# Optimization experiments

Measured on AMD Instinct MI355X. Metric: run time of the kernel, lower is better.

The kernel has to match this reference:

```python
import jax, jax.numpy as jnp
import numpy as np
import math

N_HEAD = 16

def _rope(x):
    # x: [B, H, T, D], D even; interleaved-pair rotation as in the torch code
    B, H, T, D = x.shape
    theta = 10000.0 ** (-2.0 * jnp.arange(D // 2, dtype=x.dtype) / D)  # [D/2]
    pos = jnp.arange(T, dtype=x.dtype)[:, None]                        # [T,1]
    ang = pos * theta[None, :]                                          # [T, D/2]
    sin, cos = jnp.sin(ang), jnp.cos(ang)
    x1, x2 = x[..., ::2], x[..., 1::2]
    x1r = x1 * cos - x2 * sin
    x2r = x1 * sin + x2 * cos
    # re-interleave
    out = jnp.stack([x1r, x2r], axis=-1).reshape(B, H, T, D)
    return out

def setup_inputs() -> dict:
    key = jax.random.key(0)
    ks = jax.random.split(key, 3)
    B, T, C = 4, 2048, 1024
    x = jax.random.normal(ks[0], (B, T, C), dtype=jnp.float32)
    W_qkv = jax.random.normal(ks[1], (C, 3 * C), dtype=jnp.float32) * (1.0 / math.sqrt(C))
    b_qkv = jnp.zeros((3 * C,), dtype=jnp.float32)
    W_proj = jax.random.normal(ks[2], (C, C), dtype=jnp.float32) * (1.0 / math.sqrt(C))
    b_proj = jnp.zeros((C,), dtype=jnp.float32)
    return {"x": x, "W_qkv": W_qkv, "b_qkv": b_qkv, "W_proj": W_proj, "b_proj": b_proj}

def reference(x, W_qkv, b_qkv, W_proj, b_proj):
    B, T, C = x.shape
    H = N_HEAD
    D = C // H
    qkv = x @ W_qkv + b_qkv                      # [B,T,3C]
    q, k, v = jnp.split(qkv, 3, axis=-1)
    def to_heads(t):
        return t.reshape(B, T, H, D).transpose(0, 2, 1, 3)  # [B,H,T,D]
    q, k, v = to_heads(q), to_heads(k), to_heads(v)
    q = _rope(q)
    k = _rope(k)
    att = jnp.einsum('bhqd,bhkd->bhqk', q, k) * (1.0 / math.sqrt(D))
    mask = jnp.tril(jnp.ones((T, T), dtype=bool))
    att = jnp.where(mask[None, None, :, :], att, -jnp.inf)
    att = jax.nn.softmax(att, axis=-1)
    y = jnp.einsum('bhqk,bhkd->bhqd', att, v)    # [B,H,T,D]
    y = y.transpose(0, 2, 1, 3).reshape(B, T, C)
    return y @ W_proj + b_proj
```

## Files before the change

### kernel.cpp

```cpp
#include <hip/hip_runtime.h>
#include <cstddef>

#define B_DIM 4
#define T_DIM 2048
#define C_DIM 1024
#define H_DIM 16
#define D_DIM 64
#define C3_DIM 3072

typedef __attribute__((ext_vector_type(8))) _Float16 f16x8;
typedef __attribute__((ext_vector_type(4))) _Float16 f16x4;
typedef __attribute__((ext_vector_type(4))) float f32x4;

typedef const __attribute__((address_space(1))) unsigned int* gptr_t;
typedef __attribute__((address_space(3))) unsigned int* lptr_t;

#define QSCALE 0.180336850073f
#define NTHETA 0.41524101186f

__global__ __launch_bounds__(256) void prep(
    const float* __restrict__ x, _Float16* __restrict__ xh,
    const float* __restrict__ Wq, _Float16* __restrict__ Wqt,
    const float* __restrict__ Wp, _Float16* __restrict__ Wpt)
{
    __shared__ float tile[64][65];
    const int z = blockIdx.x, tid = threadIdx.x;

    if (z < 8192) {
        size_t i = (size_t)z * 1024 + tid * 4;
        float4 v = *(const float4*)&x[i];
        f16x4 o = { (_Float16)v.x, (_Float16)v.y, (_Float16)v.z, (_Float16)v.w };
        *(f16x4*)&xh[i] = o;
        return;
    }

    const float* W;
    _Float16* Wt;
    int N, idx;
    if (z < 8960) { W = Wq; Wt = Wqt; N = C3_DIM; idx = z - 8192; }
    else          { W = Wp; Wt = Wpt; N = C_DIM;  idx = z - 8960; }
    const int K = C_DIM;
    const int nblk = N / 64;
    const int n0 = (idx % nblk) * 64, k0 = (idx / nblk) * 64;

    const int tx = tid & 15, ty = tid >> 4;
#pragma unroll
    for (int it = 0; it < 4; ++it) {
        int r = it * 16 + ty;
        *(float4*)&tile[r][tx * 4] =
            *(const float4*)&W[(size_t)(k0 + r) * N + n0 + tx * 4];
    }
    __syncthreads();
    int c = tid >> 2, t0 = (tid & 3) * 16;
    __align__(16) _Float16 tmp[16];
#pragma unroll
    for (int j = 0; j < 16; ++j) tmp[j] = (_Float16)tile[t0 + j][c];
    _Float16* o = Wt + (size_t)(n0 + c) * K + k0 + t0;
    *(f16x8*)o = *(f16x8*)&tmp[0];
    *(f16x8*)(o + 8) = *(f16x8*)&tmp[8];
}

__global__ __launch_bounds__(256) void gemm_qkv(
    const _Float16* __restrict__ A, const _Float16* __restrict__ Bt,
    const float* __restrict__ bias,
    _Float16* __restrict__ Qb, _Float16* __restrict__ Kb, _Float16* __restrict__ Vt)
{
    __shared__ __align__(16) _Float16 Af[8][64][8];
    __shared__ __align__(16) _Float16 Bf[8][64][8];
    const int tid = threadIdx.x;
    const int lane = tid & 63, w = tid >> 6;
    const int lm = lane & 15, lq = lane >> 4;
    const int wm = w >> 1, wn = w & 1;
    const int m0 = blockIdx.y * 128, n0 = blockIdx.x * 128;
    const int K = C_DIM;

    const _Float16* a0 = A + (size_t)(m0 + w * 32 + lm) * K + lq * 8;
    const _Float16* a1 = a0 + (size_t)16 * K;
    const _Float16* b0 = Bt + (size_t)(n0 + w * 32 + lm) * K + lq * 8;
    const _Float16* b1 = b0 + (size_t)16 * K;

    f32x4 acc[4][4];
#pragma unroll
    for (int i = 0; i < 4; ++i)
#pragma unroll
        for (int j = 0; j < 4; ++j) acc[i][j] = (f32x4){0.f, 0.f, 0.f, 0.f};

    const bool is_v = (n0 >= 2 * C_DIM);

    if (!is_v) {
        for (int k0 = 0; k0 < K; k0 += 32) {
            __syncthreads();
            __builtin_amdgcn_global_load_lds((gptr_t)(const void*)(a0 + k0),
                (lptr_t)(void*)&Af[w * 2 + 0][0][0], 16, 0, 0);
            __builtin_amdgcn_global_load_lds((gptr_t)(const void*)(a1 + k0),
                (lptr_t)(void*)&Af[w * 2 + 1][0][0], 16, 0, 0);
            __builtin_amdgcn_global_load_lds((gptr_t)(const void*)(b0 + k0),
                (lptr_t)(void*)&Bf[w * 2 + 0][0][0], 16, 0, 0);
            __builtin_amdgcn_global_load_lds((gptr_t)(const void*)(b1 + k0),
                (lptr_t)(void*)&Bf[w * 2 + 1][0][0], 16, 0, 0);
            __syncthreads();
            f16x8 av[4], bv[4];
#pragma unroll
            for (int i = 0; i < 4; ++i) {
                av[i] = *(const f16x8*)&Af[wm * 4 + i][lane][0];
                bv[i] = *(const f16x8*)&Bf[wn * 4 + i][lane][0];
            }
#pragma unroll
            for (int i = 0; i < 4; ++i)
#pragma unroll
                for (int j = 0; j < 4; ++j)
                    acc[i][j] = __builtin_amdgcn_mfma_f32_16x16x32_f16(
                        bv[j], av[i], acc[i][j], 0, 0, 0);
        }

        const bool is_q = (n0 < C_DIM);
        const float scale = is_q ? QSCALE : 1.0f;
        _Float16* dstbase = is_q ? Qb : Kb;
#pragma unroll
        for (int j = 0; j < 4; ++j) {
            int col = n0 + wn * 64 + j * 16 + lq * 4;
            int d0 = col & 63;
            int h = (col & (C_DIM - 1)) >> 6;
            float4 b4 = *(const float4*)&bias[col];
            float th0 = exp2f(-NTHETA * (float)(d0 >> 1));
            float th1 = exp2f(-NTHETA * (float)((d0 >> 1) + 1));
#pragma unroll
            for (int i = 0; i < 4; ++i) {
                int tg = m0 + wm * 64 + i * 16 + lm;
                int bb = tg >> 11, tl = tg & (T_DIM - 1);
                float v0 = acc[i][j][0] + b4.x;
                float v1 = acc[i][j][1] + b4.y;
                float v2 = acc[i][j][2] + b4.z;
                float v3 = acc[i][j][3] + b4.w;
                float s0, c0, s1, c1;
                __sincosf((float)tl * th0, &s0, &c0);
                __sincosf((float)tl * th1, &s1, &c1);
                f16x4 o = { (_Float16)((v0 * c0 - v1 * s0) * scale),
                            (_Float16)((v0 * s0 + v1 * c0) * scale),
                            (_Float16)((v2 * c1 - v3 * s1) * scale),
                            (_Float16)((v2 * s1 + v3 * c1) * scale) };
                *(f16x4*)&dstbase[((size_t)(bb * 16 + h) * T_DIM + tl) * 64 + d0] = o;
            }
        }
    } else {
        for (int k0 = 0; k0 < K; k0 += 32) {
            __syncthreads();
            __builtin_amdgcn_global_load_lds((gptr_t)(const void*)(a0 + k0),
                (lptr_t)(void*)&Af[w * 2 + 0][0][0], 16, 0, 0);
            __builtin_amdgcn_global_load_lds((gptr_t)(const void*)(a1 + k0),
                (lptr_t)(void*)&Af[w * 2 + 1][0][0], 16, 0, 0);
            __builtin_amdgcn_global_load_lds((gptr_t)(const void*)(b0 + k0),
                (lptr_t)(void*)&Bf[w * 2 + 0][0][0], 16, 0, 0);
            __builtin_amdgcn_global_load_lds((gptr_t)(const void*)(b1 + k0),
                (lptr_t)(void*)&Bf[w * 2 + 1][0][0], 16, 0, 0);
            __syncthreads();
            f16x8 av[4], bv[4];
#pragma unroll
            for (int i = 0; i < 4; ++i) {
                av[i] = *(const f16x8*)&Af[wm * 4 + i][lane][0];
                bv[i] = *(const f16x8*)&Bf[wn * 4 + i][lane][0];
            }
#pragma unroll
            for (int i = 0; i < 4; ++i)
#pragma unroll
                for (int j = 0; j < 4; ++j)
                    acc[i][j] = __builtin_amdgcn_mfma_f32_16x16x32_f16(
                        av[i], bv[j], acc[i][j], 0, 0, 0);
        }

#pragma unroll
        for (int i = 0; i < 4; ++i) {
            int t4 = m0 + wm * 64 + i * 16 + lq * 4;
            int bb = t4 >> 11, tl = t4 & (T_DIM - 1);
#pragma unroll
            for (int j = 0; j < 4; ++j) {
                int col = n0 + wn * 64 + j * 16 + lm;
                int dfull = col - 2 * C_DIM;
                int h = dfull >> 6, d = dfull & 63;
                float bc = bias[col];
                f16x4 o = { (_Float16)(acc[i][j][0] + bc),
                            (_Float16)(acc[i][j][1] + bc),
                            (_Float16)(acc[i][j][2] + bc),
                            (_Float16)(acc[i][j][3] + bc) };
                *(f16x4*)&Vt[((size_t)(bb * 16 + h) * 64 + d) * T_DIM + tl] = o;
            }
        }
    }
}

template <bool OUT_HALF>
__global__ __launch_bounds__(256) void gemm_bt(
    const _Float16* __restrict__ A, const _Float16* __restrict__ Bt,
    const float* __restrict__ bias, void* __restrict__ Cout,
    int M, int N, int K)
{
    __shared__ __align__(16) _Float16 Af[8][64][8];
    __shared__ __align__(16) _Float16 Bf[8][64][8];
    const int tid = threadIdx.x;
    const int lane = tid & 63, w = tid >> 6;
    const int lm = lane & 15, lq = lane >> 4;
    const int wm = w >> 1, wn = w & 1;
    const int m0 = blockIdx.y * 128, n0 = blockIdx.x * 128;

    const _Float16* a0 = A + (size_t)(m0 + w * 32 + lm) * K + lq * 8;
    const _Float16* a1 = a0 + (size_t)16 * K;
    const _Float16* b0 = Bt + (size_t)(n0 + w * 32 + lm) * K + lq * 8;
    const _Float16* b1 = b0 + (size_t)16 * K;

    f32x4 acc[4][4];
#pragma unroll
    for (int i = 0; i < 4; ++i)
#pragma unroll
        for (int j = 0; j < 4; ++j) acc[i][j] = (f32x4){0.f, 0.f, 0.f, 0.f};

    for (int k0 = 0; k0 < K; k0 += 32) {
        __syncthreads();
        __builtin_amdgcn_global_load_lds((gptr_t)(const void*)(a0 + k0),
            (lptr_t)(void*)&Af[w * 2 + 0][0][0], 16, 0, 0);
        __builtin_amdgcn_global_load_lds((gptr_t)(const void*)(a1 + k0),
            (lptr_t)(void*)&Af[w * 2 + 1][0][0], 16, 0, 0);
        __builtin_amdgcn_global_load_lds((gptr_t)(const void*)(b0 + k0),
            (lptr_t)(void*)&Bf[w * 2 + 0][0][0], 16, 0, 0);
        __builtin_amdgcn_global_load_lds((gptr_t)(const void*)(b1 + k0),
            (lptr_t)(void*)&Bf[w * 2 + 1][0][0], 16, 0, 0);
        __syncthreads();

        f16x8 av[4], bv[4];
#pragma unroll
        for (int i = 0; i < 4; ++i) {
            av[i] = *(const f16x8*)&Af[wm * 4 + i][lane][0];
            bv[i] = *(const f16x8*)&Bf[wn * 4 + i][lane][0];
        }
#pragma unroll
        for (int i = 0; i < 4; ++i)
#pragma unroll
            for (int j = 0; j < 4; ++j)
                acc[i][j] = __builtin_amdgcn_mfma_f32_16x16x32_f16(
                    bv[j], av[i], acc[i][j], 0, 0, 0);
    }

#pragma unroll
    for (int i = 0; i < 4; ++i) {
        size_t row = (size_t)(m0 + wm * 64 + i * 16 + lm);
#pragma unroll
        for (int j = 0; j < 4; ++j) {
            int col = n0 + wn * 64 + j * 16 + lq * 4;
            float4 b4 = *(const float4*)&bias[col];
            float v0 = acc[i][j][0] + b4.x;
            float v1 = acc[i][j][1] + b4.y;
            float v2 = acc[i][j][2] + b4.z;
            float v3 = acc[i][j][3] + b4.w;
            if (OUT_HALF) {
                f16x4 o = { (_Float16)v0, (_Float16)v1, (_Float16)v2, (_Float16)v3 };
                *(f16x4*)&((_Float16*)Cout)[row * N + col] = o;
            } else {
                float4 o = make_float4(v0, v1, v2, v3);
                *(float4*)&((float*)Cout)[row * N + col] = o;
            }
        }
    }
}

__global__ __launch_bounds__(256) void attn_mfma(
    const _Float16* __restrict__ Qb, const _Float16* __restrict__ Kb,
    const _Float16* __restrict__ Vt, _Float16* __restrict__ yb)
{
    __shared__ __align__(16) _Float16 Kf[8][64][8];
    __shared__ __align__(16) _Float16 Vf[8][64][8];
    __shared__ __align__(16) _Float16 Pb[4][16][72];

    const int tid = threadIdx.x;
    const int bh = blockIdx.x;
    const int qt = 31 - blockIdx.y;
    const int b = bh >> 4, h = bh & 15;
    const int lane = tid & 63, w = tid >> 6;
    const int m = lane & 15, qq = lane >> 4;

    const _Float16* qrow = Qb +
        ((size_t)bh * T_DIM + qt * 64 + w * 16 + m) * D_DIM + qq * 8;
    f16x8 qreg[2];
    qreg[0] = *(const f16x8*)qrow;
    qreg[1] = *(const f16x8*)(qrow + 32);

    float m_i = -1e30f, l_i = 0.f;
    f32x4 acc[4];
#pragma unroll
    for (int db = 0; db < 4; ++db) acc[db] = (f32x4){0.f, 0.f, 0.f, 0.f};

    const _Float16* kg0 = Kb + (size_t)bh * T_DIM * D_DIM +
                          (size_t)(w * 16 + m) * D_DIM + qq * 8;
    const _Float16* vg0 = Vt + (size_t)bh * D_DIM * T_DIM +
                          (size_t)(w * 16 + m) * T_DIM + qq * 8;

    f16x8 kr0 = *(const f16x8*)(kg0);
    f16x8 kr1 = *(const f16x8*)(kg0 + 32);
    f16x8 vr0 = *(const f16x8*)(vg0);
    f16x8 vr1 = *(const f16x8*)(vg0 + 32);

    for (int kt = 0; kt <= qt; ++kt) {
        __syncthreads();
        *(f16x8*)&Kf[w * 2 + 0][lane][0] = kr0;
        *(f16x8*)&Kf[w * 2 + 1][lane][0] = kr1;
        *(f16x8*)&Vf[w * 2 + 0][lane][0] = vr0;
        *(f16x8*)&Vf[w * 2 + 1][lane][0] = vr1;
        __syncthreads();

        int ktn = (kt < qt) ? kt + 1 : kt;
        kr0 = *(const f16x8*)(kg0 + (size_t)ktn * 64 * D_DIM);
        kr1 = *(const f16x8*)(kg0 + (size_t)ktn * 64 * D_DIM + 32);
        vr0 = *(const f16x8*)(vg0 + ktn * 64);
        vr1 = *(const f16x8*)(vg0 + ktn * 64 + 32);

        f32x4 sv[4];
#pragma unroll
        for (int nb = 0; nb < 4; ++nb) {
            f32x4 s = (f32x4){0.f, 0.f, 0.f, 0.f};
            s = __builtin_amdgcn_mfma_f32_16x16x32_f16(
                *(const f16x8*)&Kf[nb * 2 + 0][lane][0], qreg[0], s, 0, 0, 0);
            s = __builtin_amdgcn_mfma_f32_16x16x32_f16(
                *(const f16x8*)&Kf[nb * 2 + 1][lane][0], qreg[1], s, 0, 0, 0);
            sv[nb] = s;
        }

        if (kt == qt) {
            int qlocal = w * 16 + m;
#pragma unroll
            for (int nb = 0; nb < 4; ++nb) {
                int tb = nb * 16 + qq * 4;
#pragma unroll
                for (int r = 0; r < 4; ++r)
                    if (tb + r > qlocal) sv[nb][r] = -1e30f;
            }
        }

        float mt0 = fmaxf(fmaxf(sv[0][0], sv[0][1]), fmaxf(sv[0][2], sv[0][3]));
        float mt1 = fmaxf(fmaxf(sv[1][0], sv[1][1]), fmaxf(sv[1][2], sv[1][3]));
        float mt2 = fmaxf(fmaxf(sv[2][0], sv[2][1]), fmaxf(sv[2][2], sv[2][3]));
        float mt3 = fmaxf(fmaxf(sv[3][0], sv[3][1]), fmaxf(sv[3][2], sv[3][3]));
        float mt = fmaxf(fmaxf(mt0, mt1), fmaxf(mt2, mt3));
        mt = fmaxf(mt, __shfl_xor(mt, 16));
        mt = fmaxf(mt, __shfl_xor(mt, 32));
        float mnew = fmaxf(m_i, mt);
        float alpha = exp2f(m_i - mnew);
        float ll = 0.f;
#pragma unroll
        for (int nb = 0; nb < 4; ++nb) {
            float p0 = exp2f(sv[nb][0] - mnew);
            float p1 = exp2f(sv[nb][1] - mnew);
            float p2 = exp2f(sv[nb][2] - mnew);
            float p3 = exp2f(sv[nb][3] - mnew);
            sv[nb][0] = p0; sv[nb][1] = p1; sv[nb][2] = p2; sv[nb][3] = p3;
            ll += (p0 + p1) + (p2 + p3);
        }
        ll += __shfl_xor(ll, 16);
        ll += __shfl_xor(ll, 32);
        l_i = l_i * alpha + ll;
        m_i = mnew;
#pragma unroll
        for (int db = 0; db < 4; ++db) {
            acc[db][0] *= alpha; acc[db][1] *= alpha;
            acc[db][2] *= alpha; acc[db][3] *= alpha;
        }

#pragma unroll
        for (int nb = 0; nb < 4; ++nb) {
            f16x4 pv = { (_Float16)sv[nb][0], (_Float16)sv[nb][1],
                         (_Float16)sv[nb][2], (_Float16)sv[nb][3] };
            *(f16x4*)&Pb[w][m][nb * 16 + qq * 4] = pv;
        }

        f16x8 pf0 = *(const f16x8*)&Pb[w][m][0 * 32 + qq * 8];
        f16x8 pf1 = *(const f16x8*)&Pb[w][m][1 * 32 + qq * 8];

#pragma unroll
        for (int db = 0; db < 4; ++db) {
            acc[db] = __builtin_amdgcn_mfma_f32_16x16x32_f16(
                *(const f16x8*)&Vf[db * 2 + 0][lane][0], pf0, acc[db], 0, 0, 0);
            acc[db] = __builtin_amdgcn_mfma_f32_16x16x32_f16(
                *(const f16x8*)&Vf[db * 2 + 1][lane][0], pf1, acc[db], 0, 0, 0);
        }
    }

    float inv = 1.0f / l_i;
    _Float16* yrow = yb + (size_t)(b * T_DIM + qt * 64 + w * 16 + m) * C_DIM +
                     h * D_DIM + qq * 4;
#pragma unroll
    for (int db = 0; db < 4; ++db) {
        f16x4 o = { (_Float16)(acc[db][0] * inv), (_Float16)(acc[db][1] * inv),
                    (_Float16)(acc[db][2] * inv), (_Float16)(acc[db][3] * inv) };
        *(f16x4*)(yrow + db * 16) = o;
    }
}

extern "C" void kernel_launch(void* const* d_in, const int* in_sizes, int n_in,
                              void* d_out, int out_size, void* d_ws, size_t ws_size,
                              hipStream_t stream)
{
    const float* x     = (const float*)d_in[0];
    const float* Wqkv  = (const float*)d_in[1];
    const float* bqkv  = (const float*)d_in[2];
    const float* Wproj = (const float*)d_in[3];
    const float* bproj = (const float*)d_in[4];
    float* out = (float*)d_out;

    char* ws = (char*)d_ws;
    _Float16* xh  = (_Float16*)(ws);
    _Float16* yh  = (_Float16*)(ws + 16777216ull);
    _Float16* Qb  = (_Float16*)(ws + 33554432ull);
    _Float16* Kb  = (_Float16*)(ws + 50331648ull);
    _Float16* Vt  = (_Float16*)(ws + 67108864ull);
    _Float16* Wqt = (_Float16*)(ws + 83886080ull);
    _Float16* Wpt = (_Float16*)(ws + 90177536ull);

    dim3 blk(256);

    prep<<<dim3(9216), blk, 0, stream>>>(x, xh, Wqkv, Wqt, Wproj, Wpt);

    gemm_qkv<<<dim3(C3_DIM / 128, (B_DIM * T_DIM) / 128), blk, 0, stream>>>(
        xh, Wqt, bqkv, Qb, Kb, Vt);

    attn_mfma<<<dim3(B_DIM * H_DIM, T_DIM / 64), blk, 0, stream>>>(
        Qb, Kb, Vt, yh);

    gemm_bt<false><<<dim3(C_DIM / 128, (B_DIM * T_DIM) / 128), blk, 0, stream>>>(
        yh, Wpt, bproj, out, B_DIM * T_DIM, C_DIM, C_DIM);
}
```

Baseline: 319.1 us.

## Double-buffer LDS tiles and widen K-step to 64 in QKV and projection GEMMs

Both GEMM kernels now stage two K-slices of 32 (64 total) per iteration into a double-buffered LDS array. The next tile's global-to-LDS loads are issued before computing on the current buffer, and there is one barrier per 64-wide step instead of two per 32-wide step. The goal is to hide global load latency behind MFMA work and cut synchronisation overhead. LDS use per block grows fourfold (to 64 KB total), which may lower occupancy.

```diff
diff --git a/kernel.cpp b/kernel.cpp
--- a/kernel.cpp
+++ b/kernel.cpp
@@ -60,13 +60,55 @@
     *(f16x8*)(o + 8) = *(f16x8*)&tmp[8];
 }
 
+#define STAGE8(BUF, KK)                                                       \
+    do {                                                                      \
+        __builtin_amdgcn_global_load_lds((gptr_t)(const void*)(ag + (KK)),    \
+            (lptr_t)(void*)&Af[BUF][0][w * 2 + 0][0][0], 16, 0, 0);           \
+        __builtin_amdgcn_global_load_lds((gptr_t)(const void*)(ag + (KK) + 16 * K), \
+            (lptr_t)(void*)&Af[BUF][0][w * 2 + 1][0][0], 16, 0, 0);           \
+        __builtin_amdgcn_global_load_lds((gptr_t)(const void*)(ag + (KK) + 32), \
+            (lptr_t)(void*)&Af[BUF][1][w * 2 + 0][0][0], 16, 0, 0);           \
+        __builtin_amdgcn_global_load_lds((gptr_t)(const void*)(ag + (KK) + 32 + 16 * K), \
+            (lptr_t)(void*)&Af[BUF][1][w * 2 + 1][0][0], 16, 0, 0);           \
+        __builtin_amdgcn_global_load_lds((gptr_t)(const void*)(bg + (KK)),    \
+            (lptr_t)(void*)&Bf[BUF][0][w * 2 + 0][0][0], 16, 0, 0);           \
+        __builtin_amdgcn_global_load_lds((gptr_t)(const void*)(bg + (KK) + 16 * K), \
+            (lptr_t)(void*)&Bf[BUF][0][w * 2 + 1][0][0], 16, 0, 0);           \
+        __builtin_amdgcn_global_load_lds((gptr_t)(const void*)(bg + (KK) + 32), \
+            (lptr_t)(void*)&Bf[BUF][1][w * 2 + 0][0][0], 16, 0, 0);           \
+        __builtin_amdgcn_global_load_lds((gptr_t)(const void*)(bg + (KK) + 32 + 16 * K), \
+            (lptr_t)(void*)&Bf[BUF][1][w * 2 + 1][0][0], 16, 0, 0);           \
+    } while (0)
+
+#define COMPUTE64(CUR, SWAPPED)                                               \
+    do {                                                                      \
+        _Pragma("unroll")                                                     \
+        for (int s = 0; s < 2; ++s) {                                         \
+            f16x8 av[4], bv[4];                                               \
+            _Pragma("unroll")                                                 \
+            for (int i = 0; i < 4; ++i) {                                     \
+                av[i] = *(const f16x8*)&Af[CUR][s][wm * 4 + i][lane][0];      \
+                bv[i] = *(const f16x8*)&Bf[CUR][s][wn * 4 + i][lane][0];      \
+            }                                                                 \
+            _Pragma("unroll")                                                 \
+            for (int i = 0; i < 4; ++i)                                       \
+                _Pragma("unroll")                                             \
+                for (int j = 0; j < 4; ++j)                                   \
+                    acc[i][j] = (SWAPPED)                                     \
+                        ? __builtin_amdgcn_mfma_f32_16x16x32_f16(             \
+                              bv[j], av[i], acc[i][j], 0, 0, 0)               \
+                        : __builtin_amdgcn_mfma_f32_16x16x32_f16(             \
+                              av[i], bv[j], acc[i][j], 0, 0, 0);              \
+        }                                                                     \
+    } while (0)
+
 __global__ __launch_bounds__(256) void gemm_qkv(
     const _Float16* __restrict__ A, const _Float16* __restrict__ Bt,
     const float* __restrict__ bias,
     _Float16* __restrict__ Qb, _Float16* __restrict__ Kb, _Float16* __restrict__ Vt)
 {
-    __shared__ __align__(16) _Float16 Af[8][64][8];
-    __shared__ __align__(16) _Float16 Bf[8][64][8];
+    __shared__ __align__(16) _Float16 Af[2][2][8][64][8];
+    __shared__ __align__(16) _Float16 Bf[2][2][8][64][8];
     const int tid = threadIdx.x;
     const int lane = tid & 63, w = tid >> 6;
     const int lm = lane & 15, lq = lane >> 4;
@@ -74,10 +116,8 @@
     const int m0 = blockIdx.y * 128, n0 = blockIdx.x * 128;
     const int K = C_DIM;
 
-    const _Float16* a0 = A + (size_t)(m0 + w * 32 + lm) * K + lq * 8;
-    const _Float16* a1 = a0 + (size_t)16 * K;
-    const _Float16* b0 = Bt + (size_t)(n0 + w * 32 + lm) * K + lq * 8;
-    const _Float16* b1 = b0 + (size_t)16 * K;
+    const _Float16* ag = A + (size_t)(m0 + w * 32 + lm) * K + lq * 8;
+    const _Float16* bg = Bt + (size_t)(n0 + w * 32 + lm) * K + lq * 8;
 
     f32x4 acc[4][4];
 #pragma unroll
@@ -88,30 +128,16 @@
     const bool is_v = (n0 >= 2 * C_DIM);
 
     if (!is_v) {
-        for (int k0 = 0; k0 < K; k0 += 32) {
+        STAGE8(0, 0);
+        __syncthreads();
+        int cur = 0;
+        for (int kt = 0; kt < K / 64 - 1; ++kt) {
+            STAGE8(cur ^ 1, (kt + 1) * 64);
+            COMPUTE64(cur, true);
             __syncthreads();
-            __builtin_amdgcn_global_load_lds((gptr_t)(const void*)(a0 + k0),
-                (lptr_t)(void*)&Af[w * 2 + 0][0][0], 16, 0, 0);
-            __builtin_amdgcn_global_load_lds((gptr_t)(const void*)(a1 + k0),
-                (lptr_t)(void*)&Af[w * 2 + 1][0][0], 16, 0, 0);
-            __builtin_amdgcn_global_load_lds((gptr_t)(const void*)(b0 + k0),
-                (lptr_t)(void*)&Bf[w * 2 + 0][0][0], 16, 0, 0);
-            __builtin_amdgcn_global_load_lds((gptr_t)(const void*)(b1 + k0),
-                (lptr_t)(void*)&Bf[w * 2 + 1][0][0], 16, 0, 0);
-            __syncthreads();
-            f16x8 av[4], bv[4];
-#pragma unroll
-            for (int i = 0; i < 4; ++i) {
-                av[i] = *(const f16x8*)&Af[wm * 4 + i][lane][0];
-                bv[i] = *(const f16x8*)&Bf[wn * 4 + i][lane][0];
-            }
-#pragma unroll
-            for (int i = 0; i < 4; ++i)
-#pragma unroll
-                for (int j = 0; j < 4; ++j)
-                    acc[i][j] = __builtin_amdgcn_mfma_f32_16x16x32_f16(
-                        bv[j], av[i], acc[i][j], 0, 0, 0);
-        }
+            cur ^= 1;
+        }
+        COMPUTE64(cur, true);
 
         const bool is_q = (n0 < C_DIM);
         const float scale = is_q ? QSCALE : 1.0f;
@@ -143,30 +169,16 @@
             }
         }
     } else {
-        for (int k0 = 0; k0 < K; k0 += 32) {
+        STAGE8(0, 0);
+        __syncthreads();
+        int cur = 0;
+        for (int kt = 0; kt < K / 64 - 1; ++kt) {
+            STAGE8(cur ^ 1, (kt + 1) * 64);
+            COMPUTE64(cur, false);
             __syncthreads();
-            __builtin_amdgcn_global_load_lds((gptr_t)(const void*)(a0 + k0),
-                (lptr_t)(void*)&Af[w * 2 + 0][0][0], 16, 0, 0);
-            __builtin_amdgcn_global_load_lds((gptr_t)(const void*)(a1 + k0),
-                (lptr_t)(void*)&Af[w * 2 + 1][0][0], 16, 0, 0);
-            __builtin_amdgcn_global_load_lds((gptr_t)(const void*)(b0 + k0),
-                (lptr_t)(void*)&Bf[w * 2 + 0][0][0], 16, 0, 0);
-            __builtin_amdgcn_global_load_lds((gptr_t)(const void*)(b1 + k0),
-                (lptr_t)(void*)&Bf[w * 2 + 1][0][0], 16, 0, 0);
-            __syncthreads();
-            f16x8 av[4], bv[4];
-#pragma unroll
-            for (int i = 0; i < 4; ++i) {
-                av[i] = *(const f16x8*)&Af[wm * 4 + i][lane][0];
-                bv[i] = *(const f16x8*)&Bf[wn * 4 + i][lane][0];
-            }
-#pragma unroll
-            for (int i = 0; i < 4; ++i)
-#pragma unroll
-                for (int j = 0; j < 4; ++j)
-                    acc[i][j] = __builtin_amdgcn_mfma_f32_16x16x32_f16(
-                        av[i], bv[j], acc[i][j], 0, 0, 0);
-        }
+            cur ^= 1;
+        }
+        COMPUTE64(cur, false);
 
 #pragma unroll
         for (int i = 0; i < 4; ++i) {
@@ -194,18 +206,16 @@
     const float* __restrict__ bias, void* __restrict__ Cout,
     int M, int N, int K)
 {
-    __shared__ __align__(16) _Float16 Af[8][64][8];
-    __shared__ __align__(16) _Float16 Bf[8][64][8];
+    __shared__ __align__(16) _Float16 Af[2][2][8][64][8];
+    __shared__ __align__(16) _Float16 Bf[2][2][8][64][8];
     const int tid = threadIdx.x;
     const int lane = tid & 63, w = tid >> 6;
     const int lm = lane & 15, lq = lane >> 4;
     const int wm = w >> 1, wn = w & 1;
     const int m0 = blockIdx.y * 128, n0 = blockIdx.x * 128;
 
-    const _Float16* a0 = A + (size_t)(m0 + w * 32 + lm) * K + lq * 8;
-    const _Float16* a1 = a0 + (size_t)16 * K;
-    const _Float16* b0 = Bt + (size_t)(n0 + w * 32 + lm) * K + lq * 8;
-    const _Float16* b1 = b0 + (size_t)16 * K;
+    const _Float16* ag = A + (size_t)(m0 + w * 32 + lm) * K + lq * 8;
+    const _Float16* bg = Bt + (size_t)(n0 + w * 32 + lm) * K + lq * 8;
 
     f32x4 acc[4][4];
 #pragma unroll
@@ -213,31 +223,16 @@
 #pragma unroll
         for (int j = 0; j < 4; ++j) acc[i][j] = (f32x4){0.f, 0.f, 0.f, 0.f};
 
-    for (int k0 = 0; k0 < K; k0 += 32) {
+    STAGE8(0, 0);
+    __syncthreads();
+    int cur = 0;
+    for (int kt = 0; kt < K / 64 - 1; ++kt) {
+        STAGE8(cur ^ 1, (kt + 1) * 64);
+        COMPUTE64(cur, true);
         __syncthreads();
-        __builtin_amdgcn_global_load_lds((gptr_t)(const void*)(a0 + k0),
-            (lptr_t)(void*)&Af[w * 2 + 0][0][0], 16, 0, 0);
-        __builtin_amdgcn_global_load_lds((gptr_t)(const void*)(a1 + k0),
-            (lptr_t)(void*)&Af[w * 2 + 1][0][0], 16, 0, 0);
-        __builtin_amdgcn_global_load_lds((gptr_t)(const void*)(b0 + k0),
-            (lptr_t)(void*)&Bf[w * 2 + 0][0][0], 16, 0, 0);
-        __builtin_amdgcn_global_load_lds((gptr_t)(const void*)(b1 + k0),
-            (lptr_t)(void*)&Bf[w * 2 + 1][0][0], 16, 0, 0);
-        __syncthreads();
-
-        f16x8 av[4], bv[4];
-#pragma unroll
-        for (int i = 0; i < 4; ++i) {
-            av[i] = *(const f16x8*)&Af[wm * 4 + i][lane][0];
-            bv[i] = *(const f16x8*)&Bf[wn * 4 + i][lane][0];
-        }
-#pragma unroll
-        for (int i = 0; i < 4; ++i)
-#pragma unroll
-            for (int j = 0; j < 4; ++j)
-                acc[i][j] = __builtin_amdgcn_mfma_f32_16x16x32_f16(
-                    bv[j], av[i], acc[i][j], 0, 0, 0);
-    }
+        cur ^= 1;
+    }
+    COMPUTE64(cur, true);
 
 #pragma unroll
     for (int i = 0; i < 4; ++i) {
```

Result: slower. 334.7 us (+4.9%).
